# Kernel tuning notes

Hardware: AMD Instinct MI355X
Metric: run time of the kernel (lower is better)

Reference implementation:

```python
import jax, jax.numpy as jnp
import numpy as np

HIDDEN = 32
FEATURES = 16
LABELS = 4
T = 8
N = 40000
E = 640000
D_IN = FEATURES + LABELS + HIDDEN + 1  # GATv2Conv input dim = 53


def setup_inputs() -> dict:
    key = jax.random.key(0)
    ks = jax.random.split(key, 16)
    x = jax.random.normal(ks[0], (T, N, FEATURES), dtype=jnp.float32)
    mask = (jax.random.uniform(ks[1], (N,)) < 0.7).astype(jnp.float32)
    labels = jax.random.normal(ks[2], (N, LABELS), dtype=jnp.float32)
    edge_index = jax.random.randint(ks[3], (2, E), 0, N, dtype=jnp.int32)
    edge_weight = jax.random.uniform(ks[4], (E,), dtype=jnp.float32)
    s = 1.0 / np.sqrt(D_IN)
    # 4 GATv2Conv layers stacked: 0=reset, 1=update, 2=cell, 3=final
    Wl = jax.random.normal(ks[5], (4, HIDDEN, D_IN), dtype=jnp.float32) * s
    bl = jnp.zeros((4, HIDDEN), dtype=jnp.float32)
    Wr = jax.random.normal(ks[6], (4, HIDDEN, D_IN), dtype=jnp.float32) * s
    br = jnp.zeros((4, HIDDEN), dtype=jnp.float32)
    att = jax.random.normal(ks[7], (4, HIDDEN), dtype=jnp.float32) * (1.0 / np.sqrt(HIDDEN))
    bconv = jnp.zeros((4, HIDDEN), dtype=jnp.float32)
    W1 = jax.random.normal(ks[8], (FEATURES, HIDDEN), dtype=jnp.float32) * (1.0 / np.sqrt(HIDDEN))
    b1 = jnp.zeros((FEATURES,), dtype=jnp.float32)
    W2 = jax.random.normal(ks[9], (FEATURES, 2 * HIDDEN), dtype=jnp.float32) * (1.0 / np.sqrt(2 * HIDDEN))
    b2 = jnp.zeros((FEATURES,), dtype=jnp.float32)
    return {"x": x, "mask": mask, "labels": labels, "edge_index": edge_index,
            "edge_weight": edge_weight, "Wl": Wl, "bl": bl, "Wr": Wr, "br": br,
            "att": att, "bconv": bconv, "W1": W1, "b1": b1, "W2": W2, "b2": b2}


def gatv2(xin, src, dst, Wl, bl, Wr, br, att, bconv):
    # GATv2Conv, heads=1, add_self_loops=False (edge_weight unused: lin_edge is None)
    xl = xin @ Wl.T + bl          # [N, H] source transform (message)
    xr = xin @ Wr.T + br          # [N, H] target transform
    z = jax.nn.leaky_relu(xl[src] + xr[dst], 0.2)  # [E, H]
    e = z @ att                   # [E] attention logits
    m = jax.ops.segment_max(e, dst, num_segments=N)
    a = jnp.exp(e - m[dst])
    den = jax.ops.segment_sum(a, dst, num_segments=N)[dst]
    a = a / jnp.where(den > 0, den, 1.0)
    out = jax.ops.segment_sum(a[:, None] * xl[src], dst, num_segments=N)
    return out + bconv


def reference(x, mask, labels, edge_index, edge_weight, Wl, bl, Wr, br, att, bconv, W1, b1, W2, b2):
    src, dst = edge_index[0], edge_index[1]
    mcol = mask[:, None]                       # [N, 1] float, concatenated as a feature
    mbool = mcol > 0.5                         # [N, 1] bool, used for where()
    masked_input = jnp.where(mbool[None], x, 0.0)  # [T, N, F]
    hidden0 = jnp.ones((N, HIDDEN), dtype=x.dtype)
    x2_0 = masked_input[0]

    def step(carry, xt):
        hidden, x2 = carry
        ft = jnp.concatenate([x2, mcol, labels], axis=1)        # [N, F+1+L]
        inp = jnp.concatenate([ft, hidden], axis=1)             # [N, D_IN]
        reset = jax.nn.sigmoid(gatv2(inp, src, dst, Wl[0], bl[0], Wr[0], br[0], att[0], bconv[0]))
        update = jax.nn.sigmoid(gatv2(inp, src, dst, Wl[1], bl[1], Wr[1], br[1], att[1], bconv[1]))
        cin = jnp.concatenate([ft, reset * hidden], axis=1)
        cell = jnp.tanh(gatv2(cin, src, dst, Wl[2], bl[2], Wr[2], br[2], att[2], bconv[2]))
        hidden = update * hidden + (1.0 - update) * cell        # (dropout inactive: eval mode)
        y1 = hidden @ W1.T + b1
        x1 = jnp.where(mbool, xt, y1)
        ft2 = jnp.concatenate([x1, mcol, hidden, labels], axis=1)  # [N, D_IN]
        s = jax.nn.relu(gatv2(ft2, src, dst, Wl[3], bl[3], Wr[3], br[3], att[3], bconv[3]))
        y2 = jnp.concatenate([s, hidden], axis=1) @ W2.T + b2
        x2_new = jnp.where(mbool, xt, y2)
        return (hidden, x2_new), x2_new

    _, out = jax.lax.scan(step, (hidden0, x2_0), masked_input)
    return out  # [T, N, F]
```

## Files before the change

kernel.cpp:

```cpp
#include <hip/hip_runtime.h>
#include <math.h>

#define NN   40000
#define EE   640000
#define HID  32
#define FEAT 16
#define LAB  4
#define TT   8
#define DIN  53
#define WD   (HID * DIN)


__device__ __forceinline__ unsigned short f2bf(float f) {
    unsigned int u = __float_as_uint(f);
    unsigned int r = u + 0x7fffu + ((u >> 16) & 1u);
    return (unsigned short)(r >> 16);
}
__device__ __forceinline__ float bflo(unsigned int u) { return __uint_as_float(u << 16); }
__device__ __forceinline__ float bfhi(unsigned int u) { return __uint_as_float(u & 0xffff0000u); }
__device__ __forceinline__ void unpack8(uint4 u, float* v) {
    v[0] = bflo(u.x); v[1] = bfhi(u.x);
    v[2] = bflo(u.y); v[3] = bfhi(u.y);
    v[4] = bflo(u.z); v[5] = bfhi(u.z);
    v[6] = bflo(u.w); v[7] = bfhi(u.w);
}


__global__ __launch_bounds__(256) void zero_i32(int* __restrict__ p, int n) {
    int i = blockIdx.x * 256 + threadIdx.x;
    if (i < n) p[i] = 0;
}

__global__ __launch_bounds__(256) void hist_kernel(const int* __restrict__ dst,
                                                   int* __restrict__ deg) {
    int e = blockIdx.x * 256 + threadIdx.x;
    if (e < EE) atomicAdd(&deg[dst[e]], 1);
}

__global__ __launch_bounds__(1024) void scan_kernel(const int* __restrict__ deg,
                                                    int* __restrict__ row_ptr) {
    __shared__ int wsum[16];
    __shared__ int chunk_total;
    int tid = threadIdx.x;
    int lane = tid & 63, wv = tid >> 6;
    int carry = 0;
    if (tid == 0) row_ptr[0] = 0;
    for (int base = 0; base < NN; base += 1024) {
        int i = base + tid;
        int v = (i < NN) ? deg[i] : 0;
        #pragma unroll
        for (int o = 1; o < 64; o <<= 1) {
            int t = __shfl_up(v, o);
            if (lane >= o) v += t;
        }
        if (lane == 63) wsum[wv] = v;
        __syncthreads();
        if (tid < 16) {
            int s = wsum[tid];
            #pragma unroll
            for (int o = 1; o < 16; o <<= 1) {
                int t = __shfl_up(s, o);
                if (tid >= o) s += t;
            }
            wsum[tid] = s;
            if (tid == 15) chunk_total = s;
        }
        __syncthreads();
        int woff = (wv == 0) ? 0 : wsum[wv - 1];
        if (i < NN) row_ptr[i + 1] = carry + woff + v;
        carry += chunk_total;
        __syncthreads();
    }
}

__global__ __launch_bounds__(256) void scatter_kernel(const int* __restrict__ src,
                                                      const int* __restrict__ dst,
                                                      const int* __restrict__ row_ptr,
                                                      int* __restrict__ cursor,
                                                      int* __restrict__ csr_src) {
    int e = blockIdx.x * 256 + threadIdx.x;
    if (e < EE) {
        int d = dst[e];
        int pos = atomicAdd(&cursor[d], 1);
        csr_src[row_ptr[d] + pos] = src[e];
    }
}

__global__ __launch_bounds__(256) void sort_kernel(const int* __restrict__ row_ptr,
                                                   int* __restrict__ csr_src) {
    int n = blockIdx.x * 256 + threadIdx.x;
    if (n < NN) {
        int beg = row_ptr[n], end = row_ptr[n + 1];
        for (int i = beg + 1; i < end; ++i) {
            int key = csr_src[i];
            int j = i - 1;
            while (j >= beg && csr_src[j] > key) {
                csr_src[j + 1] = csr_src[j];
                --j;
            }
            csr_src[j + 1] = key;
        }
    }
}


__global__ __launch_bounds__(256) void init_kernel(const float* __restrict__ x0,
                                                   const float* __restrict__ mask,
                                                   float* __restrict__ hidden,
                                                   float* __restrict__ x2) {
    int i = blockIdx.x * 256 + threadIdx.x;
    if (i < NN * HID) hidden[i] = 1.0f;
    if (i < NN * FEAT) {
        int node = i >> 4;
        x2[i] = (mask[node] > 0.5f) ? x0[i] : 0.0f;
    }
}


__global__ __launch_bounds__(256) void dense01_kernel(const float* __restrict__ feat,
                                                      const float* __restrict__ mask,
                                                      const float* __restrict__ labels,
                                                      const float* __restrict__ hsrc,
                                                      const float* __restrict__ Wl,
                                                      const float* __restrict__ bl,
                                                      const float* __restrict__ Wr,
                                                      const float* __restrict__ br,
                                                      unsigned short* __restrict__ xl01h,
                                                      float* __restrict__ xr01) {
    __shared__ float W_s[4 * WD];
    __shared__ float inp_s[8][DIN];
    for (int idx = threadIdx.x; idx < WD; idx += 256) {
        W_s[idx]          = Wl[idx];
        W_s[WD + idx]     = Wl[WD + idx];
        W_s[2 * WD + idx] = Wr[idx];
        W_s[3 * WD + idx] = Wr[WD + idx];
    }
    int ni = threadIdx.x >> 5, k = threadIdx.x & 31;
    int node = blockIdx.x * 8 + ni;
    for (int i = k; i < DIN; i += 32) {
        float v;
        if (i < 16)       v = feat[node * 16 + i];
        else if (i == 16) v = mask[node];
        else if (i < 21)  v = labels[node * 4 + (i - 17)];
        else              v = hsrc[node * 32 + (i - 21)];
        inp_s[ni][i] = v;
    }
    __syncthreads();
    float l0 = bl[k], l1 = bl[HID + k], r0 = br[k], r1 = br[HID + k];
    const float* w0 = &W_s[k * DIN];
    const float* w1 = &W_s[WD + k * DIN];
    const float* w2 = &W_s[2 * WD + k * DIN];
    const float* w3 = &W_s[3 * WD + k * DIN];
#pragma unroll
    for (int i = 0; i < DIN; ++i) {
        float xv = inp_s[ni][i];
        l0 += xv * w0[i];
        l1 += xv * w1[i];
        r0 += xv * w2[i];
        r1 += xv * w3[i];
    }
    xl01h[node * 64 + k]      = f2bf(l0);
    xl01h[node * 64 + 32 + k] = f2bf(l1);
    xr01[node * 64 + k]      = r0;
    xr01[node * 64 + 32 + k] = r1;
}


__global__ __launch_bounds__(256) void dense_kernel(const float* __restrict__ feat,
                                                    const float* __restrict__ mask,
                                                    const float* __restrict__ labels,
                                                    const float* __restrict__ hsrc,
                                                    const float* __restrict__ hmul,
                                                    const float* __restrict__ Wl,
                                                    const float* __restrict__ bl,
                                                    const float* __restrict__ Wr,
                                                    const float* __restrict__ br,
                                                    unsigned short* __restrict__ xlh,
                                                    float* __restrict__ xr) {
    __shared__ float Wl_s[WD];
    __shared__ float Wr_s[WD];
    __shared__ float inp_s[8][DIN];
    for (int idx = threadIdx.x; idx < WD; idx += 256) {
        Wl_s[idx] = Wl[idx];
        Wr_s[idx] = Wr[idx];
    }
    int ni = threadIdx.x >> 5, k = threadIdx.x & 31;
    int node = blockIdx.x * 8 + ni;
    for (int i = k; i < DIN; i += 32) {
        float v;
        if (i < 16)       v = feat[node * 16 + i];
        else if (i == 16) v = mask[node];
        else if (i < 21)  v = labels[node * 4 + (i - 17)];
        else              v = hsrc[node * 32 + (i - 21)] * hmul[node * 32 + (i - 21)];
        inp_s[ni][i] = v;
    }
    __syncthreads();
    float al = bl[k], ar = br[k];
    const float* wlr = &Wl_s[k * DIN];
    const float* wrr = &Wr_s[k * DIN];
#pragma unroll
    for (int i = 0; i < DIN; ++i) {
        float xv = inp_s[ni][i];
        al += xv * wlr[i];
        ar += xv * wrr[i];
    }
    xlh[node * 32 + k] = f2bf(al);
    xr[node * 32 + k] = ar;
}


__device__ __forceinline__ float edge_score8(const float* v, const float* xr, const float* at) {
    float part = 0.0f;
#pragma unroll
    for (int i = 0; i < 8; ++i) {
        float z = v[i] + xr[i];
        z = (z > 0.0f) ? z : 0.2f * z;
        part += z * at[i];
    }
    part += __shfl_xor(part, 1);
    part += __shfl_xor(part, 2);
    return part;
}

__device__ __forceinline__ void online_update8(float e, float& m, float& den, float* acc,
                                               const float* v) {
    if (e > m) {
        float sc = __expf(m - e);
        den *= sc;
#pragma unroll
        for (int i = 0; i < 8; ++i) acc[i] *= sc;
        m = e;
    }
    float a = __expf(e - m);
    den += a;
#pragma unroll
    for (int i = 0; i < 8; ++i) acc[i] += a * v[i];
}

__device__ __forceinline__ void merge_full(float m, float den, const float* acc,
                                           bool ne, float* o) {
    if (ne) {
        float mt = m;
        mt = fmaxf(mt, __shfl_xor(mt, 4));
        mt = fmaxf(mt, __shfl_xor(mt, 8));
        mt = fmaxf(mt, __shfl_xor(mt, 16));
        mt = fmaxf(mt, __shfl_xor(mt, 32));
        float sc = __expf(m - mt);
        float d = den * sc;
        d += __shfl_xor(d, 4);
        d += __shfl_xor(d, 8);
        d += __shfl_xor(d, 16);
        d += __shfl_xor(d, 32);
#pragma unroll
        for (int i = 0; i < 8; ++i) {
            float t = acc[i] * sc;
            t += __shfl_xor(t, 4);
            t += __shfl_xor(t, 8);
            t += __shfl_xor(t, 16);
            t += __shfl_xor(t, 32);
            o[i] = t / d;
        }
    } else {
#pragma unroll
        for (int i = 0; i < 8; ++i) o[i] = 0.0f;
    }
}


__global__ __launch_bounds__(256) void conv01_kernel(const int* __restrict__ row_ptr,
                                                     const int* __restrict__ csr_src,
                                                     const unsigned short* __restrict__ xl01h,
                                                     const float* __restrict__ xr01,
                                                     const float* __restrict__ att,
                                                     const float* __restrict__ bconv,
                                                     float* __restrict__ g0,
                                                     float* __restrict__ g1) {
    int wid  = threadIdx.x >> 6;
    int lane = threadIdx.x & 63;
    int g = lane >> 2, j = lane & 3;
    int n = blockIdx.x * 4 + wid;
    int c0 = j * 8;
    int beg = row_ptr[n], end = row_ptr[n + 1];

    float at0v[8], at1v[8], xr0v[8], xr1v[8];
    {
        float4 a0 = *(const float4*)(att + c0);
        float4 a1 = *(const float4*)(att + c0 + 4);
        at0v[0] = a0.x; at0v[1] = a0.y; at0v[2] = a0.z; at0v[3] = a0.w;
        at0v[4] = a1.x; at0v[5] = a1.y; at0v[6] = a1.z; at0v[7] = a1.w;
        float4 b0 = *(const float4*)(att + 32 + c0);
        float4 b1 = *(const float4*)(att + 32 + c0 + 4);
        at1v[0] = b0.x; at1v[1] = b0.y; at1v[2] = b0.z; at1v[3] = b0.w;
        at1v[4] = b1.x; at1v[5] = b1.y; at1v[6] = b1.z; at1v[7] = b1.w;
        const float* xrn = xr01 + n * 64;
        float4 r0 = *(const float4*)(xrn + c0);
        float4 r1 = *(const float4*)(xrn + c0 + 4);
        xr0v[0] = r0.x; xr0v[1] = r0.y; xr0v[2] = r0.z; xr0v[3] = r0.w;
        xr0v[4] = r1.x; xr0v[5] = r1.y; xr0v[6] = r1.z; xr0v[7] = r1.w;
        float4 r2 = *(const float4*)(xrn + 32 + c0);
        float4 r3 = *(const float4*)(xrn + 32 + c0 + 4);
        xr1v[0] = r2.x; xr1v[1] = r2.y; xr1v[2] = r2.z; xr1v[3] = r2.w;
        xr1v[4] = r3.x; xr1v[5] = r3.y; xr1v[6] = r3.z; xr1v[7] = r3.w;
    }

    float m0 = -INFINITY, den0 = 0.0f, acc0[8] = {0, 0, 0, 0, 0, 0, 0, 0};
    float m1 = -INFINITY, den1 = 0.0f, acc1[8] = {0, 0, 0, 0, 0, 0, 0, 0};

    for (int p = beg + g; p < end; p += 16) {
        int s = csr_src[p];
        const unsigned short* row = xl01h + (size_t)s * 64;
        uint4 u0 = *(const uint4*)(row + c0);
        uint4 u1 = *(const uint4*)(row + 32 + c0);
        float v0[8], v1[8];
        unpack8(u0, v0);
        unpack8(u1, v1);
        float e0 = edge_score8(v0, xr0v, at0v);
        float e1 = edge_score8(v1, xr1v, at1v);
        online_update8(e0, m0, den0, acc0, v0);
        online_update8(e1, m1, den1, acc1, v1);
    }

    float o0[8], o1[8];
    bool ne = beg < end;
    merge_full(m0, den0, acc0, ne, o0);
    merge_full(m1, den1, acc1, ne, o1);

    if (g == 0) {
        const float* bc0 = bconv + c0;
        const float* bc1 = bconv + 32 + c0;
        float r0[8], r1[8];
#pragma unroll
        for (int i = 0; i < 8; ++i) {
            r0[i] = 1.0f / (1.0f + __expf(-(o0[i] + bc0[i])));
            r1[i] = 1.0f / (1.0f + __expf(-(o1[i] + bc1[i])));
        }
        float* p0 = g0 + n * 32 + c0;
        ((float4*)p0)[0] = make_float4(r0[0], r0[1], r0[2], r0[3]);
        ((float4*)p0)[1] = make_float4(r0[4], r0[5], r0[6], r0[7]);
        float* p1 = g1 + n * 32 + c0;
        ((float4*)p1)[0] = make_float4(r1[0], r1[1], r1[2], r1[3]);
        ((float4*)p1)[1] = make_float4(r1[4], r1[5], r1[6], r1[7]);
    }
}


__global__ __launch_bounds__(256) void conv2_kernel(const int* __restrict__ row_ptr,
                                                    const int* __restrict__ csr_src,
                                                    const unsigned short* __restrict__ xlh,
                                                    const float* __restrict__ xr,
                                                    const float* __restrict__ att,
                                                    const float* __restrict__ bconv,
                                                    float* __restrict__ out) {
    int wid  = threadIdx.x >> 6;
    int lane = threadIdx.x & 63;
    int g = lane >> 2, j = lane & 3;
    int n = blockIdx.x * 4 + wid;
    int c0 = j * 8;
    int beg = row_ptr[n], end = row_ptr[n + 1];

    float at[8], xrv[8];
    {
        float4 a0 = *(const float4*)(att + c0);
        float4 a1 = *(const float4*)(att + c0 + 4);
        at[0] = a0.x; at[1] = a0.y; at[2] = a0.z; at[3] = a0.w;
        at[4] = a1.x; at[5] = a1.y; at[6] = a1.z; at[7] = a1.w;
        float4 r0 = *(const float4*)(xr + n * 32 + c0);
        float4 r1 = *(const float4*)(xr + n * 32 + c0 + 4);
        xrv[0] = r0.x; xrv[1] = r0.y; xrv[2] = r0.z; xrv[3] = r0.w;
        xrv[4] = r1.x; xrv[5] = r1.y; xrv[6] = r1.z; xrv[7] = r1.w;
    }

    float m = -INFINITY, den = 0.0f, acc[8] = {0, 0, 0, 0, 0, 0, 0, 0};
    for (int p = beg + g; p < end; p += 16) {
        int s = csr_src[p];
        uint4 u = *(const uint4*)(xlh + (size_t)s * 32 + c0);
        float v[8];
        unpack8(u, v);
        float e = edge_score8(v, xrv, at);
        online_update8(e, m, den, acc, v);
    }
    float o[8];
    merge_full(m, den, acc, beg < end, o);

    if (g == 0) {
        const float* bc = bconv + c0;
        float r[8];
#pragma unroll
        for (int i = 0; i < 8; ++i) r[i] = tanhf(o[i] + bc[i]);
        float* op = out + n * 32 + c0;
        ((float4*)op)[0] = make_float4(r[0], r[1], r[2], r[3]);
        ((float4*)op)[1] = make_float4(r[4], r[5], r[6], r[7]);
    }
}


__global__ __launch_bounds__(256) void conv3_out_kernel(const int* __restrict__ row_ptr,
                                                        const int* __restrict__ csr_src,
                                                        const unsigned short* __restrict__ xlh,
                                                        const float* __restrict__ xr,
                                                        const float* __restrict__ att,
                                                        const float* __restrict__ bconv,
                                                        const float* __restrict__ hidden,
                                                        const float* __restrict__ W2,
                                                        const float* __restrict__ b2,
                                                        const float* __restrict__ x_t,
                                                        const float* __restrict__ mask,
                                                        float* __restrict__ x2,
                                                        float* __restrict__ out_t) {
    __shared__ float W2s[64 * 16];
    for (int idx = threadIdx.x; idx < 64 * 16; idx += 256) {
        int f = idx & 15, c = idx >> 4;
        W2s[c * 16 + f] = W2[f * 64 + c];
    }
    __syncthreads();

    int wid  = threadIdx.x >> 6;
    int lane = threadIdx.x & 63;
    int g = lane >> 2, j = lane & 3;
    int n = blockIdx.x * 4 + wid;
    int c0 = j * 8;
    int beg = row_ptr[n], end = row_ptr[n + 1];

    float at[8], xrv[8];
    {
        float4 a0 = *(const float4*)(att + c0);
        float4 a1 = *(const float4*)(att + c0 + 4);
        at[0] = a0.x; at[1] = a0.y; at[2] = a0.z; at[3] = a0.w;
        at[4] = a1.x; at[5] = a1.y; at[6] = a1.z; at[7] = a1.w;
        float4 r0 = *(const float4*)(xr + n * 32 + c0);
        float4 r1 = *(const float4*)(xr + n * 32 + c0 + 4);
        xrv[0] = r0.x; xrv[1] = r0.y; xrv[2] = r0.z; xrv[3] = r0.w;
        xrv[4] = r1.x; xrv[5] = r1.y; xrv[6] = r1.z; xrv[7] = r1.w;
    }

    float m = -INFINITY, den = 0.0f, acc[8] = {0, 0, 0, 0, 0, 0, 0, 0};
    for (int p = beg + g; p < end; p += 16) {
        int s = csr_src[p];
        uint4 u = *(const uint4*)(xlh + (size_t)s * 32 + c0);
        float v[8];
        unpack8(u, v);
        float e = edge_score8(v, xrv, at);
        online_update8(e, m, den, acc, v);
    }
    float o[8];
    merge_full(m, den, acc, beg < end, o);

    float r[8], hv[8];
    {
        const float* bc = bconv + c0;
#pragma unroll
        for (int i = 0; i < 8; ++i) r[i] = fmaxf(o[i] + bc[i], 0.0f);
        float4 h0 = *(const float4*)(hidden + n * 32 + c0);
        float4 h1 = *(const float4*)(hidden + n * 32 + c0 + 4);
        hv[0] = h0.x; hv[1] = h0.y; hv[2] = h0.z; hv[3] = h0.w;
        hv[4] = h1.x; hv[5] = h1.y; hv[6] = h1.z; hv[7] = h1.w;
    }

    int f = lane & 15;
    int base = lane & ~3;
    float y = b2[f];
#pragma unroll
    for (int j2 = 0; j2 < 4; ++j2) {
#pragma unroll
        for (int i = 0; i < 8; ++i) {
            float sv = __shfl(r[i], base + j2);
            float hh = __shfl(hv[i], base + j2);
            int c = j2 * 8 + i;
            y += sv * W2s[c * 16 + f] + hh * W2s[(32 + c) * 16 + f];
        }
    }
    if (lane < 16) {
        float mv = mask[n];
        float xv = x_t[n * 16 + f];
        float rr = (mv > 0.5f) ? xv : y;
        x2[n * 16 + f] = rr;
        out_t[n * 16 + f] = rr;
    }
}


__global__ __launch_bounds__(256) void update_dense3_kernel(
        const float* __restrict__ g_update, const float* __restrict__ g_cell,
        float* __restrict__ hidden,
        const float* __restrict__ x_t, const float* __restrict__ mask,
        const float* __restrict__ labels,
        const float* __restrict__ W1, const float* __restrict__ b1,
        const float* __restrict__ Wl3, const float* __restrict__ bl3,
        const float* __restrict__ Wr3, const float* __restrict__ br3,
        unsigned short* __restrict__ xlh, float* __restrict__ xr) {
    __shared__ float Wl_s[WD];
    __shared__ float Wr_s[WD];
    __shared__ float W1_s[FEAT * HID];
    __shared__ float inp_s[8][DIN];
    __shared__ float hs[8][HID + 1];
    for (int idx = threadIdx.x; idx < WD; idx += 256) {
        Wl_s[idx] = Wl3[idx];
        Wr_s[idx] = Wr3[idx];
    }
    for (int idx = threadIdx.x; idx < FEAT * HID; idx += 256) W1_s[idx] = W1[idx];
    int ni = threadIdx.x >> 5, k = threadIdx.x & 31;
    int node = blockIdx.x * 8 + ni;
    float u = g_update[node * 32 + k];
    float c = g_cell[node * 32 + k];
    float h = hidden[node * 32 + k];
    float hn = u * h + (1.0f - u) * c;
    hidden[node * 32 + k] = hn;
    hs[ni][k] = hn;
    inp_s[ni][17 + k] = hn;
    if (k == 0) inp_s[ni][16] = mask[node];
    if (k < 4)  inp_s[ni][49 + k] = labels[node * 4 + k];
    __syncthreads();
    if (k < 16) {
        float a = b1[k];
        const float* w = &W1_s[k * 32];
#pragma unroll
        for (int i = 0; i < 32; ++i) a += hs[ni][i] * w[i];
        float mv = mask[node];
        inp_s[ni][k] = (mv > 0.5f) ? x_t[node * 16 + k] : a;
    }
    __syncthreads();
    float al = bl3[k], ar = br3[k];
    const float* wl = &Wl_s[k * DIN];
    const float* wr = &Wr_s[k * DIN];
#pragma unroll
    for (int i = 0; i < DIN; ++i) {
        float xv = inp_s[ni][i];
        al += xv * wl[i];
        ar += xv * wr[i];
    }
    xlh[node * 32 + k] = f2bf(al);
    xr[node * 32 + k] = ar;
}


extern "C" void kernel_launch(void* const* d_in, const int* in_sizes, int n_in,
                              void* d_out, int out_size, void* d_ws, size_t ws_size,
                              hipStream_t stream) {
    const float* x      = (const float*)d_in[0];
    const float* mask   = (const float*)d_in[1];
    const float* labels = (const float*)d_in[2];
    const int*   src    = (const int*)d_in[3];
    const int*   dst    = src + EE;
    const float* Wl    = (const float*)d_in[5];
    const float* bl    = (const float*)d_in[6];
    const float* Wr    = (const float*)d_in[7];
    const float* br    = (const float*)d_in[8];
    const float* att   = (const float*)d_in[9];
    const float* bconv = (const float*)d_in[10];
    const float* W1    = (const float*)d_in[11];
    const float* b1    = (const float*)d_in[12];
    const float* W2    = (const float*)d_in[13];
    const float* b2    = (const float*)d_in[14];
    float* out = (float*)d_out;

    char* ws = (char*)d_ws;
    size_t off = 0;
    auto alloc = [&](size_t bytes) -> void* {
        void* p = ws + off;
        off = (off + bytes + 255) & ~(size_t)255;
        return p;
    };
    int*   row_ptr = (int*)alloc((NN + 1) * sizeof(int));
    int*   deg     = (int*)alloc(NN * sizeof(int));
    int*   csr_src = (int*)alloc(EE * sizeof(int));
    float* hidden  = (float*)alloc(NN * HID * sizeof(float));
    float* x2      = (float*)alloc(NN * FEAT * sizeof(float));
    unsigned short* xl01h = (unsigned short*)alloc(NN * 64 * sizeof(unsigned short));
    float* xr01    = (float*)alloc(NN * 64 * sizeof(float));
    unsigned short* xlh = (unsigned short*)alloc(NN * 32 * sizeof(unsigned short));
    float* xr      = (float*)alloc(NN * HID * sizeof(float));
    float* g0      = (float*)alloc(NN * HID * sizeof(float));
    float* g1      = (float*)alloc(NN * HID * sizeof(float));
    float* g2      = (float*)alloc(NN * HID * sizeof(float));

    zero_i32<<<(NN + 255) / 256, 256, 0, stream>>>(deg, NN);
    hist_kernel<<<EE / 256, 256, 0, stream>>>(dst, deg);
    scan_kernel<<<1, 1024, 0, stream>>>(deg, row_ptr);
    zero_i32<<<(NN + 255) / 256, 256, 0, stream>>>(deg, NN);
    scatter_kernel<<<EE / 256, 256, 0, stream>>>(src, dst, row_ptr, deg, csr_src);
    sort_kernel<<<(NN + 255) / 256, 256, 0, stream>>>(row_ptr, csr_src);
    init_kernel<<<NN * HID / 256, 256, 0, stream>>>(x, mask, hidden, x2);

    for (int t = 0; t < TT; ++t) {
        const float* xt = x + (size_t)t * NN * FEAT;
        float* out_t = out + (size_t)t * NN * FEAT;
        dense01_kernel<<<NN / 8, 256, 0, stream>>>(x2, mask, labels, hidden,
            Wl, bl, Wr, br, xl01h, xr01);
        conv01_kernel<<<NN / 4, 256, 0, stream>>>(row_ptr, csr_src, xl01h, xr01,
            att, bconv, g0, g1);
        dense_kernel<<<NN / 8, 256, 0, stream>>>(x2, mask, labels, hidden, g0,
            Wl + 2 * WD, bl + 2 * HID, Wr + 2 * WD, br + 2 * HID, xlh, xr);
        conv2_kernel<<<NN / 4, 256, 0, stream>>>(row_ptr, csr_src, xlh, xr,
            att + 2 * HID, bconv + 2 * HID, g2);
        update_dense3_kernel<<<NN / 8, 256, 0, stream>>>(g1, g2, hidden, xt, mask, labels,
            W1, b1, Wl + 3 * WD, bl + 3 * HID, Wr + 3 * WD, br + 3 * HID, xlh, xr);
        conv3_out_kernel<<<NN / 4, 256, 0, stream>>>(row_ptr, csr_src, xlh, xr,
            att + 3 * HID, bconv + 3 * HID, hidden, W2, b2, xt, mask, x2, out_t);
    }
}
```

Baseline: 2.176 ms.

## Amortize weight staging over 32 nodes per block and split conv01 across half-waves

The three dense kernels now process 32 nodes per block in four iterations, so the weights staged in shared memory are reused across more nodes instead of being reloaded by every 8-node block. This cuts redundant weight loads and launches a quarter as many blocks, at the cost of extra barriers and less parallelism per launch. Separately, conv01 now gives each half of a 64-lane wave one of the two attention layers, with 8 edge groups per half instead of 16 groups processing both layers. This halves per-thread registers and loads per edge, but each thread walks twice as many edges, and a new half-wave merge routine reduces only within 32 lanes.

```diff
diff --git a/kernel.cpp b/kernel.cpp
--- a/kernel.cpp
+++ b/kernel.cpp
@@ -136,33 +136,38 @@
         W_s[3 * WD + idx] = Wr[WD + idx];
     }
     int ni = threadIdx.x >> 5, k = threadIdx.x & 31;
-    int node = blockIdx.x * 8 + ni;
-    for (int i = k; i < DIN; i += 32) {
-        float v;
-        if (i < 16)       v = feat[node * 16 + i];
-        else if (i == 16) v = mask[node];
-        else if (i < 21)  v = labels[node * 4 + (i - 17)];
-        else              v = hsrc[node * 32 + (i - 21)];
-        inp_s[ni][i] = v;
-    }
-    __syncthreads();
-    float l0 = bl[k], l1 = bl[HID + k], r0 = br[k], r1 = br[HID + k];
     const float* w0 = &W_s[k * DIN];
     const float* w1 = &W_s[WD + k * DIN];
     const float* w2 = &W_s[2 * WD + k * DIN];
     const float* w3 = &W_s[3 * WD + k * DIN];
-#pragma unroll
-    for (int i = 0; i < DIN; ++i) {
-        float xv = inp_s[ni][i];
-        l0 += xv * w0[i];
-        l1 += xv * w1[i];
-        r0 += xv * w2[i];
-        r1 += xv * w3[i];
-    }
-    xl01h[node * 64 + k]      = f2bf(l0);
-    xl01h[node * 64 + 32 + k] = f2bf(l1);
-    xr01[node * 64 + k]      = r0;
-    xr01[node * 64 + 32 + k] = r1;
+    float bl0 = bl[k], bl1 = bl[HID + k], br0 = br[k], br1 = br[HID + k];
+#pragma unroll
+    for (int it = 0; it < 4; ++it) {
+        int node = blockIdx.x * 32 + it * 8 + ni;
+        __syncthreads();
+        for (int i = k; i < DIN; i += 32) {
+            float v;
+            if (i < 16)       v = feat[node * 16 + i];
+            else if (i == 16) v = mask[node];
+            else if (i < 21)  v = labels[node * 4 + (i - 17)];
+            else              v = hsrc[node * 32 + (i - 21)];
+            inp_s[ni][i] = v;
+        }
+        __syncthreads();
+        float l0 = bl0, l1 = bl1, r0 = br0, r1 = br1;
+#pragma unroll
+        for (int i = 0; i < DIN; ++i) {
+            float xv = inp_s[ni][i];
+            l0 += xv * w0[i];
+            l1 += xv * w1[i];
+            r0 += xv * w2[i];
+            r1 += xv * w3[i];
+        }
+        xl01h[node * 64 + k]      = f2bf(l0);
+        xl01h[node * 64 + 32 + k] = f2bf(l1);
+        xr01[node * 64 + k]      = r0;
+        xr01[node * 64 + 32 + k] = r1;
+    }
 }
 
 
@@ -185,27 +190,32 @@
         Wr_s[idx] = Wr[idx];
     }
     int ni = threadIdx.x >> 5, k = threadIdx.x & 31;
-    int node = blockIdx.x * 8 + ni;
-    for (int i = k; i < DIN; i += 32) {
-        float v;
-        if (i < 16)       v = feat[node * 16 + i];
-        else if (i == 16) v = mask[node];
-        else if (i < 21)  v = labels[node * 4 + (i - 17)];
-        else              v = hsrc[node * 32 + (i - 21)] * hmul[node * 32 + (i - 21)];
-        inp_s[ni][i] = v;
-    }
-    __syncthreads();
-    float al = bl[k], ar = br[k];
     const float* wlr = &Wl_s[k * DIN];
     const float* wrr = &Wr_s[k * DIN];
-#pragma unroll
-    for (int i = 0; i < DIN; ++i) {
-        float xv = inp_s[ni][i];
-        al += xv * wlr[i];
-        ar += xv * wrr[i];
-    }
-    xlh[node * 32 + k] = f2bf(al);
-    xr[node * 32 + k] = ar;
+    float blv = bl[k], brv = br[k];
+#pragma unroll
+    for (int it = 0; it < 4; ++it) {
+        int node = blockIdx.x * 32 + it * 8 + ni;
+        __syncthreads();
+        for (int i = k; i < DIN; i += 32) {
+            float v;
+            if (i < 16)       v = feat[node * 16 + i];
+            else if (i == 16) v = mask[node];
+            else if (i < 21)  v = labels[node * 4 + (i - 17)];
+            else              v = hsrc[node * 32 + (i - 21)] * hmul[node * 32 + (i - 21)];
+            inp_s[ni][i] = v;
+        }
+        __syncthreads();
+        float al = blv, ar = brv;
+#pragma unroll
+        for (int i = 0; i < DIN; ++i) {
+            float xv = inp_s[ni][i];
+            al += xv * wlr[i];
+            ar += xv * wrr[i];
+        }
+        xlh[node * 32 + k] = f2bf(al);
+        xr[node * 32 + k] = ar;
+    }
 }
 
 
@@ -266,6 +276,32 @@
     }
 }
 
+__device__ __forceinline__ void merge_half(float m, float den, const float* acc,
+                                           bool ne, float* o) {
+    if (ne) {
+        float mt = m;
+        mt = fmaxf(mt, __shfl_xor(mt, 4));
+        mt = fmaxf(mt, __shfl_xor(mt, 8));
+        mt = fmaxf(mt, __shfl_xor(mt, 16));
+        float sc = __expf(m - mt);
+        float d = den * sc;
+        d += __shfl_xor(d, 4);
+        d += __shfl_xor(d, 8);
+        d += __shfl_xor(d, 16);
+#pragma unroll
+        for (int i = 0; i < 8; ++i) {
+            float t = acc[i] * sc;
+            t += __shfl_xor(t, 4);
+            t += __shfl_xor(t, 8);
+            t += __shfl_xor(t, 16);
+            o[i] = t / d;
+        }
+    } else {
+#pragma unroll
+        for (int i = 0; i < 8; ++i) o[i] = 0.0f;
+    }
+}
+
 
 __global__ __launch_bounds__(256) void conv01_kernel(const int* __restrict__ row_ptr,
                                                      const int* __restrict__ csr_src,
@@ -277,69 +313,45 @@
                                                      float* __restrict__ g1) {
     int wid  = threadIdx.x >> 6;
     int lane = threadIdx.x & 63;
-    int g = lane >> 2, j = lane & 3;
+    int h  = lane >> 5;
+    int hl = lane & 31;
+    int g = hl >> 2, j = hl & 3;
     int n = blockIdx.x * 4 + wid;
     int c0 = j * 8;
     int beg = row_ptr[n], end = row_ptr[n + 1];
 
-    float at0v[8], at1v[8], xr0v[8], xr1v[8];
+    float at[8], xr[8];
     {
-        float4 a0 = *(const float4*)(att + c0);
-        float4 a1 = *(const float4*)(att + c0 + 4);
-        at0v[0] = a0.x; at0v[1] = a0.y; at0v[2] = a0.z; at0v[3] = a0.w;
-        at0v[4] = a1.x; at0v[5] = a1.y; at0v[6] = a1.z; at0v[7] = a1.w;
-        float4 b0 = *(const float4*)(att + 32 + c0);
-        float4 b1 = *(const float4*)(att + 32 + c0 + 4);
-        at1v[0] = b0.x; at1v[1] = b0.y; at1v[2] = b0.z; at1v[3] = b0.w;
-        at1v[4] = b1.x; at1v[5] = b1.y; at1v[6] = b1.z; at1v[7] = b1.w;
-        const float* xrn = xr01 + n * 64;
-        float4 r0 = *(const float4*)(xrn + c0);
-        float4 r1 = *(const float4*)(xrn + c0 + 4);
-        xr0v[0] = r0.x; xr0v[1] = r0.y; xr0v[2] = r0.z; xr0v[3] = r0.w;
-        xr0v[4] = r1.x; xr0v[5] = r1.y; xr0v[6] = r1.z; xr0v[7] = r1.w;
-        float4 r2 = *(const float4*)(xrn + 32 + c0);
-        float4 r3 = *(const float4*)(xrn + 32 + c0 + 4);
-        xr1v[0] = r2.x; xr1v[1] = r2.y; xr1v[2] = r2.z; xr1v[3] = r2.w;
-        xr1v[4] = r3.x; xr1v[5] = r3.y; xr1v[6] = r3.z; xr1v[7] = r3.w;
-    }
-
-    float m0 = -INFINITY, den0 = 0.0f, acc0[8] = {0, 0, 0, 0, 0, 0, 0, 0};
-    float m1 = -INFINITY, den1 = 0.0f, acc1[8] = {0, 0, 0, 0, 0, 0, 0, 0};
-
-    for (int p = beg + g; p < end; p += 16) {
+        float4 a0 = *(const float4*)(att + h * 32 + c0);
+        float4 a1 = *(const float4*)(att + h * 32 + c0 + 4);
+        at[0] = a0.x; at[1] = a0.y; at[2] = a0.z; at[3] = a0.w;
+        at[4] = a1.x; at[5] = a1.y; at[6] = a1.z; at[7] = a1.w;
+        float4 r0 = *(const float4*)(xr01 + n * 64 + h * 32 + c0);
+        float4 r1 = *(const float4*)(xr01 + n * 64 + h * 32 + c0 + 4);
+        xr[0] = r0.x; xr[1] = r0.y; xr[2] = r0.z; xr[3] = r0.w;
+        xr[4] = r1.x; xr[5] = r1.y; xr[6] = r1.z; xr[7] = r1.w;
+    }
+
+    float m = -INFINITY, den = 0.0f, acc[8] = {0, 0, 0, 0, 0, 0, 0, 0};
+    for (int p = beg + g; p < end; p += 8) {
         int s = csr_src[p];
-        const unsigned short* row = xl01h + (size_t)s * 64;
-        uint4 u0 = *(const uint4*)(row + c0);
-        uint4 u1 = *(const uint4*)(row + 32 + c0);
-        float v0[8], v1[8];
-        unpack8(u0, v0);
-        unpack8(u1, v1);
-        float e0 = edge_score8(v0, xr0v, at0v);
-        float e1 = edge_score8(v1, xr1v, at1v);
-        online_update8(e0, m0, den0, acc0, v0);
-        online_update8(e1, m1, den1, acc1, v1);
-    }
-
-    float o0[8], o1[8];
-    bool ne = beg < end;
-    merge_full(m0, den0, acc0, ne, o0);
-    merge_full(m1, den1, acc1, ne, o1);
-
-    if (g == 0) {
-        const float* bc0 = bconv + c0;
-        const float* bc1 = bconv + 32 + c0;
-        float r0[8], r1[8];
-#pragma unroll
-        for (int i = 0; i < 8; ++i) {
-            r0[i] = 1.0f / (1.0f + __expf(-(o0[i] + bc0[i])));
-            r1[i] = 1.0f / (1.0f + __expf(-(o1[i] + bc1[i])));
-        }
-        float* p0 = g0 + n * 32 + c0;
-        ((float4*)p0)[0] = make_float4(r0[0], r0[1], r0[2], r0[3]);
-        ((float4*)p0)[1] = make_float4(r0[4], r0[5], r0[6], r0[7]);
-        float* p1 = g1 + n * 32 + c0;
-        ((float4*)p1)[0] = make_float4(r1[0], r1[1], r1[2], r1[3]);
-        ((float4*)p1)[1] = make_float4(r1[4], r1[5], r1[6], r1[7]);
+        uint4 u = *(const uint4*)(xl01h + (size_t)s * 64 + h * 32 + c0);
+        float v[8];
+        unpack8(u, v);
+        float e = edge_score8(v, xr, at);
+        online_update8(e, m, den, acc, v);
+    }
+    float o[8];
+    merge_half(m, den, acc, beg < end, o);
+
+    if (hl < 4) {
+        const float* bc = bconv + h * 32 + c0;
+        float r[8];
+#pragma unroll
+        for (int i = 0; i < 8; ++i) r[i] = 1.0f / (1.0f + __expf(-(o[i] + bc[i])));
+        float* outp = (h ? g1 : g0) + n * 32 + c0;
+        ((float4*)outp)[0] = make_float4(r[0], r[1], r[2], r[3]);
+        ((float4*)outp)[1] = make_float4(r[4], r[5], r[6], r[7]);
     }
 }
 
@@ -499,37 +511,42 @@
     }
     for (int idx = threadIdx.x; idx < FEAT * HID; idx += 256) W1_s[idx] = W1[idx];
     int ni = threadIdx.x >> 5, k = threadIdx.x & 31;
-    int node = blockIdx.x * 8 + ni;
-    float u = g_update[node * 32 + k];
-    float c = g_cell[node * 32 + k];
-    float h = hidden[node * 32 + k];
-    float hn = u * h + (1.0f - u) * c;
-    hidden[node * 32 + k] = hn;
-    hs[ni][k] = hn;
-    inp_s[ni][17 + k] = hn;
-    if (k == 0) inp_s[ni][16] = mask[node];
-    if (k < 4)  inp_s[ni][49 + k] = labels[node * 4 + k];
-    __syncthreads();
-    if (k < 16) {
-        float a = b1[k];
-        const float* w = &W1_s[k * 32];
-#pragma unroll
-        for (int i = 0; i < 32; ++i) a += hs[ni][i] * w[i];
-        float mv = mask[node];
-        inp_s[ni][k] = (mv > 0.5f) ? x_t[node * 16 + k] : a;
-    }
-    __syncthreads();
-    float al = bl3[k], ar = br3[k];
     const float* wl = &Wl_s[k * DIN];
     const float* wr = &Wr_s[k * DIN];
-#pragma unroll
-    for (int i = 0; i < DIN; ++i) {
-        float xv = inp_s[ni][i];
-        al += xv * wl[i];
-        ar += xv * wr[i];
-    }
-    xlh[node * 32 + k] = f2bf(al);
-    xr[node * 32 + k] = ar;
+    float bl3v = bl3[k], br3v = br3[k];
+#pragma unroll
+    for (int it = 0; it < 4; ++it) {
+        int node = blockIdx.x * 32 + it * 8 + ni;
+        __syncthreads();
+        float u = g_update[node * 32 + k];
+        float c = g_cell[node * 32 + k];
+        float h = hidden[node * 32 + k];
+        float hn = u * h + (1.0f - u) * c;
+        hidden[node * 32 + k] = hn;
+        hs[ni][k] = hn;
+        inp_s[ni][17 + k] = hn;
+        if (k == 0) inp_s[ni][16] = mask[node];
+        if (k < 4)  inp_s[ni][49 + k] = labels[node * 4 + k];
+        __syncthreads();
+        if (k < 16) {
+            float a = b1[k];
+            const float* w = &W1_s[k * 32];
+#pragma unroll
+            for (int i = 0; i < 32; ++i) a += hs[ni][i] * w[i];
+            float mv = mask[node];
+            inp_s[ni][k] = (mv > 0.5f) ? x_t[node * 16 + k] : a;
+        }
+        __syncthreads();
+        float al = bl3v, ar = br3v;
+#pragma unroll
+        for (int i = 0; i < DIN; ++i) {
+            float xv = inp_s[ni][i];
+            al += xv * wl[i];
+            ar += xv * wr[i];
+        }
+        xlh[node * 32 + k] = f2bf(al);
+        xr[node * 32 + k] = ar;
+    }
 }
 
 
@@ -584,15 +601,15 @@
     for (int t = 0; t < TT; ++t) {
         const float* xt = x + (size_t)t * NN * FEAT;
         float* out_t = out + (size_t)t * NN * FEAT;
-        dense01_kernel<<<NN / 8, 256, 0, stream>>>(x2, mask, labels, hidden,
+        dense01_kernel<<<NN / 32, 256, 0, stream>>>(x2, mask, labels, hidden,
             Wl, bl, Wr, br, xl01h, xr01);
         conv01_kernel<<<NN / 4, 256, 0, stream>>>(row_ptr, csr_src, xl01h, xr01,
             att, bconv, g0, g1);
-        dense_kernel<<<NN / 8, 256, 0, stream>>>(x2, mask, labels, hidden, g0,
+        dense_kernel<<<NN / 32, 256, 0, stream>>>(x2, mask, labels, hidden, g0,
             Wl + 2 * WD, bl + 2 * HID, Wr + 2 * WD, br + 2 * HID, xlh, xr);
         conv2_kernel<<<NN / 4, 256, 0, stream>>>(row_ptr, csr_src, xlh, xr,
             att + 2 * HID, bconv + 2 * HID, g2);
-        update_dense3_kernel<<<NN / 8, 256, 0, stream>>>(g1, g2, hidden, xt, mask, labels,
+        update_dense3_kernel<<<NN / 32, 256, 0, stream>>>(g1, g2, hidden, xt, mask, labels,
             W1, b1, Wl + 3 * WD, bl + 3 * HID, Wr + 3 * WD, br + 3 * HID, xlh, xr);
         conv3_out_kernel<<<NN / 4, 256, 0, stream>>>(row_ptr, csr_src, xlh, xr,
             att + 3 * HID, bconv + 3 * HID, hidden, W2, b2, xt, mask, x2, out_t);
```

Result: faster. 1.926 ms (-11.5%).
